# Kernel tuning notes

Measured on AMD Instinct MI355X. Metric: run time of the kernel, lower is better.

## Reference

```python
import jax, jax.numpy as jnp
import numpy as np

B, S, D, H = 2, 2048, 1024, 16
HD = D // H  # head_dim = 64


def setup_inputs() -> dict:
    key = jax.random.key(0)
    ks = jax.random.split(key, 12)
    s = 1.0 / np.sqrt(D)
    return {
        "query": jax.random.normal(ks[0], (B, S, D), jnp.float32),
        "key": jax.random.normal(ks[1], (B, S, D), jnp.float32),
        "value": jax.random.normal(ks[2], (B, S, D), jnp.float32),
        "attention_mask": jnp.zeros((B, S, S), jnp.float32),
        "WQ_w": jax.random.normal(ks[3], (D, D), jnp.float32) * s,
        "WQ_b": jnp.zeros((D,), jnp.float32),
        "WK_w": jax.random.normal(ks[4], (D, D), jnp.float32) * s,
        "WK_b": jnp.zeros((D,), jnp.float32),
        "WV_w": jax.random.normal(ks[5], (D, D), jnp.float32) * s,
        "WV_b": jnp.zeros((D,), jnp.float32),
        "WO_w": jax.random.normal(ks[6], (D, D), jnp.float32) * s,
        "WO_b": jnp.zeros((D,), jnp.float32),
    }


def _split_heads(x):
    # [B,S,D] -> [B,H,S,HD]
    b, s, _ = x.shape
    return x.reshape(b, s, H, HD).transpose(0, 2, 1, 3)


def reference(query, key, value, attention_mask,
              WQ_w, WQ_b, WK_w, WK_b, WV_w, WV_b, WO_w, WO_b):
    Q = _split_heads(query @ WQ_w.T + WQ_b)   # [B,H,S,HD]
    K = _split_heads(key @ WK_w.T + WK_b)
    V = _split_heads(value @ WV_w.T + WV_b)
    scale = 1.0 / jnp.sqrt(jnp.float32(HD))
    scores = jnp.einsum('bhqd,bhkd->bhqk', Q, K) * scale
    scores = scores + attention_mask[:, None, :, :]
    attn = jax.nn.softmax(scores, axis=-1)    # dropout_prob=0.0 -> identity
    out = jnp.einsum('bhqk,bhkd->bhqd', attn, V)
    out = out.transpose(0, 2, 1, 3).reshape(query.shape[0], -1, D)
    return out @ WO_w.T + WO_b
```

## Files before the change

kernel.cpp:

```cpp
#include <hip/hip_runtime.h>
#include <math.h>


typedef _Float16 h8 __attribute__((ext_vector_type(8)));
typedef _Float16 h4 __attribute__((ext_vector_type(4)));
typedef float f4 __attribute__((ext_vector_type(4)));

#define MFMA16(a, b, c) __builtin_amdgcn_mfma_f32_16x16x32_f16((a), (b), (c), 0, 0, 0)
#define EXP2F(x) __builtin_amdgcn_exp2f(x)

static constexpr int Bn = 2, Sn = 2048, Dn = 1024, Hn = 16, HDn = 64;
static constexpr int Mn = Bn * Sn;
static constexpr int Kn = Dn;
static constexpr int Nn = Dn;
static constexpr int LDP = 72;
static constexpr float LOG2E = 1.4426950408889634f;

__device__ __forceinline__ void gload_lds16(const _Float16* g, _Float16* l) {
  __builtin_amdgcn_global_load_lds(
      (const __attribute__((address_space(1))) unsigned int*)g,
      (__attribute__((address_space(3))) unsigned int*)l, 16, 0, 0);
}

struct CvtJobs {
  const float* src[7];
  _Float16* dst[7];
  int n4[7];
};

__global__ __launch_bounds__(256) void cvt_kernel(CvtJobs j) {
  const int stride = gridDim.x * blockDim.x;
  const int t0 = blockIdx.x * blockDim.x + threadIdx.x;
#pragma unroll
  for (int k = 0; k < 7; ++k) {
    const float4* __restrict__ s = (const float4*)j.src[k];
    h4* __restrict__ d = (h4*)j.dst[k];
    const int n = j.n4[k];
    for (int i = t0; i < n; i += stride) {
      const float4 f = s[i];
      h4 h;
      h[0] = (_Float16)f.x; h[1] = (_Float16)f.y;
      h[2] = (_Float16)f.z; h[3] = (_Float16)f.w;
      d[i] = h;
    }
  }
}

struct QkvArgs {
  const _Float16* X[3];
  const _Float16* W[3];
  const float* bias[3];
  _Float16* out[3];
};

__global__ __launch_bounds__(256) void gemm_qkv(QkvArgs args) {
  const int z = blockIdx.z;
  const _Float16* __restrict__ X = args.X[z];
  const _Float16* __restrict__ W = args.W[z];
  const float* __restrict__ bias = args.bias[z];
  _Float16* __restrict__ out = args.out[z];

  __shared__ _Float16 As[128 * 64];
  __shared__ _Float16 Bs[128 * 64];

  const int t = threadIdx.x;
  const int lane = t & 63, wv = t >> 6;
  const int l15 = lane & 15, quad = lane >> 4;
  const int wm = (wv >> 1) * 64, wn = (wv & 1) * 64;
  const int n0 = blockIdx.x * 128, m0 = blockIdx.y * 128;

  f4 acc[4][4];
#pragma unroll
  for (int i = 0; i < 4; ++i)
#pragma unroll
    for (int j = 0; j < 4; ++j) {
      f4 zz = {0.f, 0.f, 0.f, 0.f};
      acc[i][j] = zz;
    }

  const int srow = lane >> 3, scol = (lane & 7) * 8;

  for (int k0 = 0; k0 < Kn; k0 += 64) {
    __syncthreads();
#pragma unroll
    for (int u = 0; u < 4; ++u) {
      const int s = wv * 4 + u;
      const int row = s * 8 + srow;
      gload_lds16(X + (size_t)(m0 + row) * Kn + k0 + scol, As + s * 512);
      gload_lds16(W + (size_t)(n0 + row) * Kn + k0 + scol, Bs + s * 512);
    }
    __syncthreads();
#pragma unroll
    for (int kk = 0; kk < 64; kk += 32) {
      h8 af[4], bfr[4];
#pragma unroll
      for (int i = 0; i < 4; ++i)
        af[i] = *(const h8*)&As[(wm + i * 16 + l15) * 64 + kk + quad * 8];
#pragma unroll
      for (int j = 0; j < 4; ++j)
        bfr[j] = *(const h8*)&Bs[(wn + j * 16 + l15) * 64 + kk + quad * 8];
#pragma unroll
      for (int i = 0; i < 4; ++i)
#pragma unroll
        for (int j = 0; j < 4; ++j)
          acc[i][j] = MFMA16(af[i], bfr[j], acc[i][j]);
    }
  }

  const float osc = (z == 0) ? (0.125f * LOG2E) : 1.0f;
  if (z != 2) {
#pragma unroll
    for (int j = 0; j < 4; ++j) {
      const int n = n0 + wn + j * 16 + l15;
      const float bvs = bias[n] * osc;
      const int hh = n >> 6, hd = n & 63;
#pragma unroll
      for (int i = 0; i < 4; ++i) {
        const int mb = m0 + wm + i * 16 + quad * 4;
        const int bb = mb >> 11;
#pragma unroll
        for (int r = 0; r < 4; ++r) {
          const int ss = (mb + r) & (Sn - 1);
          out[(((size_t)(bb * Hn + hh)) * Sn + ss) * HDn + hd] =
              (_Float16)(acc[i][j][r] * osc + bvs);
        }
      }
    }
  } else {
#pragma unroll
    for (int j = 0; j < 4; ++j) {
      const int n = n0 + wn + j * 16 + l15;
      const float bv = bias[n];
      const int hh = n >> 6, hd = n & 63;
#pragma unroll
      for (int i = 0; i < 4; ++i) {
        const int mb = m0 + wm + i * 16 + quad * 4;
        const int bb = mb >> 11, ss = mb & (Sn - 1);
        h4 hv;
#pragma unroll
        for (int r = 0; r < 4; ++r) hv[r] = (_Float16)(acc[i][j][r] + bv);
        *(h4*)(out + (((size_t)(bb * Hn + hh)) * HDn + hd) * Sn + ss) = hv;
      }
    }
  }
}

__global__ __launch_bounds__(256) void gemm_o(const _Float16* __restrict__ X,
                                              const _Float16* __restrict__ W,
                                              const float* __restrict__ bias,
                                              float* __restrict__ out) {
  __shared__ _Float16 As[128 * 64];
  __shared__ _Float16 Bs[128 * 64];

  const int t = threadIdx.x;
  const int lane = t & 63, wv = t >> 6;
  const int l15 = lane & 15, quad = lane >> 4;
  const int wm = (wv >> 1) * 64, wn = (wv & 1) * 64;
  const int n0 = blockIdx.x * 128, m0 = blockIdx.y * 128;

  f4 acc[4][4];
#pragma unroll
  for (int i = 0; i < 4; ++i)
#pragma unroll
    for (int j = 0; j < 4; ++j) {
      f4 zz = {0.f, 0.f, 0.f, 0.f};
      acc[i][j] = zz;
    }

  const int srow = lane >> 3, scol = (lane & 7) * 8;

  for (int k0 = 0; k0 < Kn; k0 += 64) {
    __syncthreads();
#pragma unroll
    for (int u = 0; u < 4; ++u) {
      const int s = wv * 4 + u;
      const int row = s * 8 + srow;
      gload_lds16(X + (size_t)(m0 + row) * Kn + k0 + scol, As + s * 512);
      gload_lds16(W + (size_t)(n0 + row) * Kn + k0 + scol, Bs + s * 512);
    }
    __syncthreads();
#pragma unroll
    for (int kk = 0; kk < 64; kk += 32) {
      h8 af[4], bfr[4];
#pragma unroll
      for (int i = 0; i < 4; ++i)
        af[i] = *(const h8*)&As[(wm + i * 16 + l15) * 64 + kk + quad * 8];
#pragma unroll
      for (int j = 0; j < 4; ++j)
        bfr[j] = *(const h8*)&Bs[(wn + j * 16 + l15) * 64 + kk + quad * 8];
#pragma unroll
      for (int i = 0; i < 4; ++i)
#pragma unroll
        for (int j = 0; j < 4; ++j)
          acc[i][j] = MFMA16(af[i], bfr[j], acc[i][j]);
    }
  }

#pragma unroll
  for (int j = 0; j < 4; ++j) {
    const int n = n0 + wn + j * 16 + l15;
    const float bv = bias[n];
#pragma unroll
    for (int i = 0; i < 4; ++i) {
      const int mb = m0 + wm + i * 16 + quad * 4;
#pragma unroll
      for (int r = 0; r < 4; ++r)
        out[(size_t)(mb + r) * Nn + n] = acc[i][j][r] + bv;
    }
  }
}

__global__ __launch_bounds__(256) void attn_kernel(
    const _Float16* __restrict__ Qh,
    const _Float16* __restrict__ Kh,
    const _Float16* __restrict__ Vt,
    const float* __restrict__ mask,
    _Float16* __restrict__ out) {
  __shared__ _Float16 Kl[2][64 * 64];
  __shared__ _Float16 Vl[2][64 * 64];
  __shared__ _Float16 Pl[4 * 16 * LDP];

  const int t = threadIdx.x;
  const int w = t >> 6, lane = t & 63;
  const int l15 = lane & 15, quad = lane >> 4;

  const int bh = blockIdx.y;
  const int b = bh >> 4, h = bh & 15;
  const size_t headoff = (size_t)bh * Sn * HDn;
  const _Float16* Qp = Qh + headoff;
  const _Float16* Kp = Kh + headoff;
  const _Float16* Vp = Vt + headoff;

  const int qb = blockIdx.x * 64;
  const int q0 = qb + w * 16;
  const h8 qf0 = *(const h8*)(Qp + (size_t)(q0 + l15) * HDn + quad * 8);
  const h8 qf1 = *(const h8*)(Qp + (size_t)(q0 + l15) * HDn + 32 + quad * 8);

  const float* mrow = mask + ((size_t)b * Sn + q0 + l15) * Sn;

  float m_run = -INFINITY, l_run = 0.f;
  f4 o_acc[4];
#pragma unroll
  for (int nt = 0; nt < 4; ++nt) {
    f4 zz = {0.f, 0.f, 0.f, 0.f};
    o_acc[nt] = zz;
  }

  _Float16* Pw = &Pl[(w * 16) * LDP];

  const int r8 = lane >> 3, c8 = (lane & 7) * 8;
  auto stage = [&](int kt, int bufi) {
#pragma unroll
    for (int u = 0; u < 2; ++u) {
      const int s = w * 2 + u;
      gload_lds16(Kp + (size_t)(kt * 64 + s * 8 + r8) * HDn + c8,
                  &Kl[bufi][s * 512]);
      gload_lds16(Vp + (size_t)(s * 8 + r8) * Sn + kt * 64 + c8,
                  &Vl[bufi][s * 512]);
    }
  };

  stage(0, 0);

  for (int kt = 0; kt < Sn / 64; ++kt) {
    const int cur = kt & 1;
    __syncthreads();
    if (kt + 1 < Sn / 64) stage(kt + 1, cur ^ 1);
    const _Float16* Kc = Kl[cur];
    const _Float16* Vc = Vl[cur];

    f4 s[4];
#pragma unroll
    for (int ks = 0; ks < 4; ++ks) {
      const h8 kf0 = *(const h8*)&Kc[(ks * 16 + l15) * 64 + quad * 8];
      const h8 kf1 = *(const h8*)&Kc[(ks * 16 + l15) * 64 + 32 + quad * 8];
      f4 a = {0.f, 0.f, 0.f, 0.f};
      a = MFMA16(kf0, qf0, a);
      a = MFMA16(kf1, qf1, a);
      const float4 mv = *(const float4*)(mrow + kt * 64 + ks * 16 + quad * 4);
#pragma unroll
      for (int r = 0; r < 4; ++r)
        s[ks][r] = fmaf(((const float*)&mv)[r], LOG2E, a[r]);
    }

    float mx = s[0][0];
#pragma unroll
    for (int ks = 0; ks < 4; ++ks)
#pragma unroll
      for (int r = 0; r < 4; ++r) mx = fmaxf(mx, s[ks][r]);
    mx = fmaxf(mx, __shfl_xor(mx, 16));
    mx = fmaxf(mx, __shfl_xor(mx, 32));
    const float nm = fmaxf(m_run, mx);
    const float alpha = EXP2F(m_run - nm);
    m_run = nm;
    float sm = 0.f;
#pragma unroll
    for (int ks = 0; ks < 4; ++ks)
#pragma unroll
      for (int r = 0; r < 4; ++r) {
        s[ks][r] = EXP2F(s[ks][r] - nm);
        sm += s[ks][r];
      }
    sm += __shfl_xor(sm, 16);
    sm += __shfl_xor(sm, 32);
    l_run = l_run * alpha + sm;
#pragma unroll
    for (int nt = 0; nt < 4; ++nt)
#pragma unroll
      for (int r = 0; r < 4; ++r) o_acc[nt][r] *= alpha;

#pragma unroll
    for (int ks = 0; ks < 4; ++ks) {
      h4 pv;
#pragma unroll
      for (int r = 0; r < 4; ++r) pv[r] = (_Float16)s[ks][r];
      *(h4*)&Pw[l15 * LDP + ks * 16 + quad * 4] = pv;
    }

#pragma unroll
    for (int kk = 0; kk < 64; kk += 32) {
      const h8 pf = *(const h8*)&Pw[l15 * LDP + kk + quad * 8];
#pragma unroll
      for (int nt = 0; nt < 4; ++nt) {
        const h8 vf = *(const h8*)&Vc[(nt * 16 + l15) * 64 + kk + quad * 8];
        o_acc[nt] = MFMA16(vf, pf, o_acc[nt]);
      }
    }
  }

  const float rl = 1.0f / l_run;
#pragma unroll
  for (int nt = 0; nt < 4; ++nt) {
    h4 ov;
#pragma unroll
    for (int r = 0; r < 4; ++r) ov[r] = (_Float16)(o_acc[nt][r] * rl);
    *(h4*)&Pw[l15 * LDP + nt * 16 + quad * 4] = ov;
  }
  const int qr = lane >> 2;
  const int seg = (lane & 3) * 16;
  const int qg = q0 + qr;
  _Float16* dst = out + ((size_t)b * Sn + qg) * Dn + h * 64 + seg;
  *(uint4*)dst = *(const uint4*)&Pw[qr * LDP + seg];
  *(uint4*)(dst + 8) = *(const uint4*)&Pw[qr * LDP + seg + 8];
}

extern "C" void kernel_launch(void* const* d_in, const int* in_sizes, int n_in,
                              void* d_out, int out_size, void* d_ws, size_t ws_size,
                              hipStream_t stream) {
  const float* q = (const float*)d_in[0];
  const float* k = (const float*)d_in[1];
  const float* v = (const float*)d_in[2];
  const float* mask = (const float*)d_in[3];
  const float* WQ = (const float*)d_in[4];
  const float* bQ = (const float*)d_in[5];
  const float* WK = (const float*)d_in[6];
  const float* bK = (const float*)d_in[7];
  const float* WV = (const float*)d_in[8];
  const float* bV = (const float*)d_in[9];
  const float* WO = (const float*)d_in[10];
  const float* bO = (const float*)d_in[11];

  _Float16* ws = (_Float16*)d_ws;
  const size_t MD = (size_t)Mn * Dn;
  const size_t DD = (size_t)Dn * Dn;
  _Float16* qh  = ws;
  _Float16* kh  = ws + MD;
  _Float16* vh  = ws + 2 * MD;
  _Float16* WQh = ws + 3 * MD;
  _Float16* WKh = WQh + DD;
  _Float16* WVh = WKh + DD;
  _Float16* WOh = WVh + DD;
  _Float16* Qh  = ws + 3 * MD + 4 * DD;
  _Float16* Kh  = Qh + MD;
  _Float16* Vt  = Kh + MD;
  _Float16* AO  = qh;

  CvtJobs cj;
  cj.src[0] = q;  cj.dst[0] = qh;  cj.n4[0] = (int)(MD / 4);
  cj.src[1] = k;  cj.dst[1] = kh;  cj.n4[1] = (int)(MD / 4);
  cj.src[2] = v;  cj.dst[2] = vh;  cj.n4[2] = (int)(MD / 4);
  cj.src[3] = WQ; cj.dst[3] = WQh; cj.n4[3] = (int)(DD / 4);
  cj.src[4] = WK; cj.dst[4] = WKh; cj.n4[4] = (int)(DD / 4);
  cj.src[5] = WV; cj.dst[5] = WVh; cj.n4[5] = (int)(DD / 4);
  cj.src[6] = WO; cj.dst[6] = WOh; cj.n4[6] = (int)(DD / 4);
  cvt_kernel<<<1024, 256, 0, stream>>>(cj);

  QkvArgs ga;
  ga.X[0] = qh; ga.W[0] = WQh; ga.bias[0] = bQ; ga.out[0] = Qh;
  ga.X[1] = kh; ga.W[1] = WKh; ga.bias[1] = bK; ga.out[1] = Kh;
  ga.X[2] = vh; ga.W[2] = WVh; ga.bias[2] = bV; ga.out[2] = Vt;
  gemm_qkv<<<dim3(Nn / 128, Mn / 128, 3), 256, 0, stream>>>(ga);

  attn_kernel<<<dim3(Sn / 64, Bn * Hn), 256, 0, stream>>>(Qh, Kh, Vt, mask, AO);

  gemm_o<<<dim3(Nn / 128, Mn / 128), 256, 0, stream>>>(AO, WOh, bO, (float*)d_out);
}
```

Before: 370.4 us.

## Split attention KV range across two wave groups per block and merge

The attention kernel now runs 512 threads per block, with two groups of four waves each processing half of the key/value sequence for the same 64 queries. Their partial softmax states are merged through shared memory at the end. The async global-to-LDS double buffering is replaced by synchronous loads into padded LDS tiles with two barriers per iteration. The goal is more waves in flight per query tile to hide latency, at the cost of losing load/compute overlap and adding a merge step.

```diff
diff --git a/kernel.cpp b/kernel.cpp
--- a/kernel.cpp
+++ b/kernel.cpp
@@ -210,19 +210,20 @@
   }
 }
 
-__global__ __launch_bounds__(256) void attn_kernel(
+__global__ __launch_bounds__(512) void attn_kernel(
     const _Float16* __restrict__ Qh,
     const _Float16* __restrict__ Kh,
     const _Float16* __restrict__ Vt,
     const float* __restrict__ mask,
     _Float16* __restrict__ out) {
-  __shared__ _Float16 Kl[2][64 * 64];
-  __shared__ _Float16 Vl[2][64 * 64];
-  __shared__ _Float16 Pl[4 * 16 * LDP];
+  __shared__ _Float16 smem[4 * 64 * LDP];
+  __shared__ _Float16 Pl[8 * 16 * LDP];
 
   const int t = threadIdx.x;
   const int w = t >> 6, lane = t & 63;
   const int l15 = lane & 15, quad = lane >> 4;
+  const int g = w >> 2;
+  const int wq = w & 3;
 
   const int bh = blockIdx.y;
   const int b = bh >> 4, h = bh & 15;
@@ -232,13 +233,14 @@
   const _Float16* Vp = Vt + headoff;
 
   const int qb = blockIdx.x * 64;
-  const int q0 = qb + w * 16;
+  const int q0 = qb + wq * 16;
   const h8 qf0 = *(const h8*)(Qp + (size_t)(q0 + l15) * HDn + quad * 8);
   const h8 qf1 = *(const h8*)(Qp + (size_t)(q0 + l15) * HDn + 32 + quad * 8);
 
-  const float* mrow = mask + ((size_t)b * Sn + q0 + l15) * Sn;
-
-  float m_run = -INFINITY, l_run = 0.f;
+  const int kbase = g * (Sn / 2);
+  const float* mrow = mask + ((size_t)b * Sn + q0 + l15) * Sn + kbase;
+
+  float m_run = -INFINITY, l_part = 0.f;
   f4 o_acc[4];
 #pragma unroll
   for (int nt = 0; nt < 4; ++nt) {
@@ -246,34 +248,30 @@
     o_acc[nt] = zz;
   }
 
+  _Float16* Kg = smem + g * (64 * LDP);
+  _Float16* Vg = smem + (2 + g) * (64 * LDP);
   _Float16* Pw = &Pl[(w * 16) * LDP];
 
-  const int r8 = lane >> 3, c8 = (lane & 7) * 8;
-  auto stage = [&](int kt, int bufi) {
+  const int tg = t & 255;
+
+  for (int kt = 0; kt < (Sn / 2) / 64; ++kt) {
+    __syncthreads();
 #pragma unroll
     for (int u = 0; u < 2; ++u) {
-      const int s = w * 2 + u;
-      gload_lds16(Kp + (size_t)(kt * 64 + s * 8 + r8) * HDn + c8,
-                  &Kl[bufi][s * 512]);
-      gload_lds16(Vp + (size_t)(s * 8 + r8) * Sn + kt * 64 + c8,
-                  &Vl[bufi][s * 512]);
-    }
-  };
-
-  stage(0, 0);
-
-  for (int kt = 0; kt < Sn / 64; ++kt) {
-    const int cur = kt & 1;
-    __syncthreads();
-    if (kt + 1 < Sn / 64) stage(kt + 1, cur ^ 1);
-    const _Float16* Kc = Kl[cur];
-    const _Float16* Vc = Vl[cur];
+      const int c = tg + u * 256;
+      const int row = c >> 3, c8 = (c & 7) * 8;
+      *(uint4*)&Kg[row * LDP + c8] =
+          *(const uint4*)(Kp + (size_t)(kbase + kt * 64 + row) * HDn + c8);
+      *(uint4*)&Vg[row * LDP + c8] =
+          *(const uint4*)(Vp + (size_t)row * Sn + kbase + kt * 64 + c8);
+    }
+    __syncthreads();
 
     f4 s[4];
 #pragma unroll
     for (int ks = 0; ks < 4; ++ks) {
-      const h8 kf0 = *(const h8*)&Kc[(ks * 16 + l15) * 64 + quad * 8];
-      const h8 kf1 = *(const h8*)&Kc[(ks * 16 + l15) * 64 + 32 + quad * 8];
+      const h8 kf0 = *(const h8*)&Kg[(ks * 16 + l15) * LDP + quad * 8];
+      const h8 kf1 = *(const h8*)&Kg[(ks * 16 + l15) * LDP + 32 + quad * 8];
       f4 a = {0.f, 0.f, 0.f, 0.f};
       a = MFMA16(kf0, qf0, a);
       a = MFMA16(kf1, qf1, a);
@@ -301,9 +299,7 @@
         s[ks][r] = EXP2F(s[ks][r] - nm);
         sm += s[ks][r];
       }
-    sm += __shfl_xor(sm, 16);
-    sm += __shfl_xor(sm, 32);
-    l_run = l_run * alpha + sm;
+    l_part = l_part * alpha + sm;
 #pragma unroll
     for (int nt = 0; nt < 4; ++nt)
 #pragma unroll
@@ -322,26 +318,51 @@
       const h8 pf = *(const h8*)&Pw[l15 * LDP + kk + quad * 8];
 #pragma unroll
       for (int nt = 0; nt < 4; ++nt) {
-        const h8 vf = *(const h8*)&Vc[(nt * 16 + l15) * 64 + kk + quad * 8];
+        const h8 vf = *(const h8*)&Vg[(nt * 16 + l15) * LDP + kk + quad * 8];
         o_acc[nt] = MFMA16(vf, pf, o_acc[nt]);
       }
     }
   }
 
-  const float rl = 1.0f / l_run;
-#pragma unroll
-  for (int nt = 0; nt < 4; ++nt) {
-    h4 ov;
-#pragma unroll
-    for (int r = 0; r < 4; ++r) ov[r] = (_Float16)(o_acc[nt][r] * rl);
-    *(h4*)&Pw[l15 * LDP + nt * 16 + quad * 4] = ov;
-  }
-  const int qr = lane >> 2;
-  const int seg = (lane & 3) * 16;
-  const int qg = q0 + qr;
-  _Float16* dst = out + ((size_t)b * Sn + qg) * Dn + h * 64 + seg;
-  *(uint4*)dst = *(const uint4*)&Pw[qr * LDP + seg];
-  *(uint4*)(dst + 8) = *(const uint4*)&Pw[qr * LDP + seg + 8];
+  l_part += __shfl_xor(l_part, 16);
+  l_part += __shfl_xor(l_part, 32);
+
+  __syncthreads();
+  float* Uex = (float*)smem;
+  float* mex = Uex + 4 * 16 * LDP;
+  float* lex = mex + 64;
+  if (g == 1) {
+#pragma unroll
+    for (int nt = 0; nt < 4; ++nt)
+      *(f4*)&Uex[wq * 16 * LDP + l15 * LDP + nt * 16 + quad * 4] = o_acc[nt];
+    if (quad == 0) {
+      mex[wq * 16 + l15] = m_run;
+      lex[wq * 16 + l15] = l_part;
+    }
+  }
+  __syncthreads();
+  if (g == 0) {
+    const float m1 = mex[wq * 16 + l15];
+    const float l1 = lex[wq * 16 + l15];
+    const float mm = fmaxf(m_run, m1);
+    const float f0 = EXP2F(m_run - mm);
+    const float f1 = EXP2F(m1 - mm);
+    const float rl = 1.0f / (f0 * l_part + f1 * l1);
+#pragma unroll
+    for (int nt = 0; nt < 4; ++nt) {
+      const f4 Ur = *(const f4*)&Uex[wq * 16 * LDP + l15 * LDP + nt * 16 + quad * 4];
+      h4 ov;
+#pragma unroll
+      for (int r = 0; r < 4; ++r)
+        ov[r] = (_Float16)((o_acc[nt][r] * f0 + Ur[r] * f1) * rl);
+      *(h4*)&Pw[l15 * LDP + nt * 16 + quad * 4] = ov;
+    }
+    const int qr = lane >> 2;
+    const int seg = (lane & 3) * 16;
+    _Float16* dst = out + ((size_t)b * Sn + q0 + qr) * Dn + h * 64 + seg;
+    *(uint4*)dst = *(const uint4*)&Pw[qr * LDP + seg];
+    *(uint4*)(dst + 8) = *(const uint4*)&Pw[qr * LDP + seg + 8];
+  }
 }
 
 extern "C" void kernel_launch(void* const* d_in, const int* in_sizes, int n_in,
@@ -391,7 +412,7 @@
   ga.X[2] = vh; ga.W[2] = WVh; ga.bias[2] = bV; ga.out[2] = Vt;
   gemm_qkv<<<dim3(Nn / 128, Mn / 128, 3), 256, 0, stream>>>(ga);
 
-  attn_kernel<<<dim3(Sn / 64, Bn * Hn), 256, 0, stream>>>(Qh, Kh, Vt, mask, AO);
+  attn_kernel<<<dim3(Sn / 64, Bn * Hn), 512, 0, stream>>>(Qh, Kh, Vt, mask, AO);
 
   gemm_o<<<dim3(Nn / 128, Mn / 128), 256, 0, stream>>>(AO, WOh, bO, (float*)d_out);
 }
```

Measured after the change: 302.2 us. -18.4%, faster.
